# Kernel optimization log

Measured on AMD Instinct MI355X. Metric: run time of the kernel, lower is better.

The kernel has to match this reference:

```python
import jax, jax.numpy as jnp
import numpy as np

# FP4 (e2m1) value table: sign bit in code>>3, magnitude in code&7
FP4 = jnp.array([0.0, 0.5, 1.0, 1.5, 2.0, 3.0, 4.0, 6.0,
                 -0.0, -0.5, -1.0, -1.5, -2.0, -3.0, -4.0, -6.0], dtype=jnp.float32)
BLOCK = 32  # MX block size: one shared E8M0 scale per 32 elements


def _unpack(packed):
    # packed: int32 holding byte values 0..255; low nibble first
    lo = packed & 0xF
    hi = (packed >> 4) & 0xF
    return jnp.stack([lo, hi], axis=-1).reshape(*packed.shape[:-1], packed.shape[-1] * 2)


def _dequant(packed, sf):
    # packed: [..., N//2] packed FP4 codes; sf: [..., N//32] E8M0 exponents
    vals = FP4[_unpack(packed)]                       # [..., N]
    n = vals.shape[-1]
    scale = jnp.exp2(sf.astype(jnp.float32) - 127.0)  # [..., N//32]
    vals = vals.reshape(*vals.shape[:-1], n // BLOCK, BLOCK) * scale[..., None]
    return vals.reshape(*scale.shape[:-1], n)


def setup_inputs() -> dict:
    key = jax.random.key(0)
    ks = jax.random.split(key, 6)
    M, IN, OUT, R = 8192, 4096, 4096, 128
    return {
        "x_q": jax.random.randint(ks[0], (M, IN // 2), 0, 256, dtype=jnp.int32),
        "scales_x": jax.random.randint(ks[1], (M, IN // BLOCK), 120, 134, dtype=jnp.int32),
        "weight": jax.random.randint(ks[2], (OUT, IN // 2), 0, 256, dtype=jnp.int32),
        "SF_w": jax.random.randint(ks[3], (OUT * IN // BLOCK,), 120, 134, dtype=jnp.int32),
        "low_rank_weight": jax.random.randint(ks[4], (OUT, R // 2), 0, 256, dtype=jnp.int32),
        "SF_low_rank_weight": jax.random.randint(ks[5], (OUT * R // BLOCK,), 120, 134, dtype=jnp.int32),
    }


def reference(x_q, scales_x, weight, SF_w, low_rank_weight, SF_low_rank_weight):
    OUT = weight.shape[0]
    IN = weight.shape[1] * 2
    R = low_rank_weight.shape[1] * 2  # 128
    # Low-rank path: first R unpacked features of x (R//2 packed bytes, R//32 scale blocks)
    x_lr = _dequant(x_q[:, :R // 2], scales_x[:, :R // BLOCK])                    # [M, R]
    W_lr = _dequant(low_rank_weight, SF_low_rank_weight.reshape(OUT, R // BLOCK))  # [OUT, R]
    out = jnp.einsum('mr,or->mo', x_lr, W_lr, preferred_element_type=jnp.float32)
    # Main 4-bit matmul fused with the low-rank correction
    x = _dequant(x_q, scales_x)                               # [M, IN]
    W = _dequant(weight, SF_w.reshape(OUT, IN // BLOCK))      # [OUT, IN]
    out = out + jnp.einsum('mi,oi->mo', x, W, preferred_element_type=jnp.float32)
    return out
```

## Files before the change

kernel.cpp:

```cpp
#include <hip/hip_runtime.h>
#include <hip/hip_bf16.h>
#include <stdint.h>


#define M_DIM 8192
#define N_DIM 4096
#define K_MAIN 4096
#define K_TOT 4224
#define NCHUNK 132
#define NT 33

#define XP_OFF   ((size_t)0)
#define WP_OFF   (XP_OFF + (size_t)NCHUNK * M_DIM * 16)
#define SXH_OFF  (WP_OFF + (size_t)NCHUNK * N_DIM * 16)
#define SWH_OFF  (SXH_OFF + (size_t)NT * 2 * M_DIM * 2)
#define WS_NEED  (SWH_OFF + (size_t)NT * 2 * N_DIM * 2)

typedef __attribute__((ext_vector_type(4))) float f32x4;
typedef __attribute__((ext_vector_type(16))) float f32x16;
typedef __attribute__((ext_vector_type(8))) short short8;
typedef __attribute__((ext_vector_type(8))) _Float16 half8;
typedef __attribute__((ext_vector_type(4))) int i32x4;
typedef __attribute__((ext_vector_type(8))) int i32x8;

#define SBAR() asm volatile("s_barrier" ::: "memory")

#define PXP_N (NCHUNK * M_DIM)
#define PWP_N (NCHUNK * N_DIM)
#define TSX_N (NT * 2 * M_DIM / 2)
#define TSW_N (NT * 2 * N_DIM / 2)
#define PACK_TOTAL (PXP_N + PWP_N + TSX_N + TSW_N)

__device__ inline unsigned pack4(i32x4 q) {
    return (q.x & 255) | ((q.y & 255) << 8) | ((q.z & 255) << 16) |
           ((unsigned)(q.w & 255) << 24);
}

__global__ __launch_bounds__(256)
void pack_kernel(const int* __restrict__ xq, const int* __restrict__ sx,
                 const int* __restrict__ w, const int* __restrict__ sfw,
                 const int* __restrict__ lrw, const int* __restrict__ sflr,
                 uint8_t* __restrict__ ws) {
    int t = blockIdx.x * 256 + threadIdx.x;
    if (t < PXP_N) {
        const int g = t >> 13;
        const int m = t & 8191;
        const int gs = (g < 128) ? g : (g - 128);
        const int* src = xq + (size_t)m * 2048 + gs * 16;
        i32x4 o;
        o.x = (int)pack4(*(const i32x4*)(src + 0));
        o.y = (int)pack4(*(const i32x4*)(src + 4));
        o.z = (int)pack4(*(const i32x4*)(src + 8));
        o.w = (int)pack4(*(const i32x4*)(src + 12));
        *(i32x4*)(ws + XP_OFF + ((size_t)g * M_DIM + m) * 16) = o;
    } else if (t < PXP_N + PWP_N) {
        const int i = t - PXP_N;
        const int g = i >> 12;
        const int n = i & 4095;
        const int* src = (g < 128) ? (w + (size_t)n * 2048 + g * 16)
                                   : (lrw + (size_t)n * 64 + (g - 128) * 16);
        i32x4 o;
        o.x = (int)pack4(*(const i32x4*)(src + 0));
        o.y = (int)pack4(*(const i32x4*)(src + 4));
        o.z = (int)pack4(*(const i32x4*)(src + 8));
        o.w = (int)pack4(*(const i32x4*)(src + 12));
        *(i32x4*)(ws + WP_OFF + ((size_t)g * N_DIM + n) * 16) = o;
    } else if (t < PXP_N + PWP_N + TSX_N) {
        int i = t - PXP_N - PWP_N;
        int plane = i >> 12;
        int kt = plane >> 1, h = plane & 1;
        int r2 = (i & 4095) << 1;
        int g0 = kt * 4 + h, g2 = g0 + 2;
        int s0 = (g0 < 128) ? g0 : g0 - 128;
        int s2 = (g2 < 128) ? g2 : g2 - 128;
        unsigned b0 = sx[(size_t)r2 * 128 + s0] & 255;
        unsigned b1 = sx[(size_t)r2 * 128 + s2] & 255;
        unsigned b2 = sx[(size_t)(r2 + 1) * 128 + s0] & 255;
        unsigned b3 = sx[(size_t)(r2 + 1) * 128 + s2] & 255;
        *(unsigned*)(ws + SXH_OFF + (size_t)i * 4) = b0 | (b1 << 8) | (b2 << 16) | (b3 << 24);
    } else if (t < PACK_TOTAL) {
        int i = t - PXP_N - PWP_N - TSX_N;
        int plane = i >> 11;
        int kt = plane >> 1, h = plane & 1;
        int r2 = (i & 2047) << 1;
        int g0 = kt * 4 + h, g2 = g0 + 2;
        unsigned b0, b1, b2, b3;
        if (g0 < 128) { b0 = sfw[(size_t)r2 * 128 + g0] & 255; b2 = sfw[(size_t)(r2 + 1) * 128 + g0] & 255; }
        else          { b0 = sflr[(size_t)r2 * 4 + (g0 - 128)] & 255; b2 = sflr[(size_t)(r2 + 1) * 4 + (g0 - 128)] & 255; }
        if (g2 < 128) { b1 = sfw[(size_t)r2 * 128 + g2] & 255; b3 = sfw[(size_t)(r2 + 1) * 128 + g2] & 255; }
        else          { b1 = sflr[(size_t)r2 * 4 + (g2 - 128)] & 255; b3 = sflr[(size_t)(r2 + 1) * 4 + (g2 - 128)] & 255; }
        *(unsigned*)(ws + SWH_OFF + (size_t)i * 4) = b0 | (b1 << 8) | (b2 << 16) | (b3 << 24);
    }
}

__device__ inline void gload_lds16(const void* g, void* l) {
    __builtin_amdgcn_global_load_lds(
        (const __attribute__((address_space(1))) unsigned int*)g,
        (__attribute__((address_space(3))) unsigned int*)l, 16, 0, 0);
}

__device__ inline i32x8 zext8(i32x4 v) {
    return i32x8{v.x, v.y, v.z, v.w, 0, 0, 0, 0};
}

__global__ __launch_bounds__(512, 2)
void l4b_mx6(const uint8_t* __restrict__ xp, const uint8_t* __restrict__ wp,
             const uint8_t* __restrict__ sxH, const uint8_t* __restrict__ swH,
             float* __restrict__ out) {
    __shared__ __align__(16) uint8_t As[2][4][256][16];
    __shared__ __align__(16) uint8_t Bs[2][4][256][16];

    const int tid = threadIdx.x;
    const int lane = tid & 63;
    const int wid = tid >> 6;
    const int wr = wid >> 2;
    const int wc = wid & 3;

    const int bid = blockIdx.x;
    const int wgid = (bid & 7) * 64 + (bid >> 3);
    const int bn = (wgid & 15) * 256;
    const int bm = (wgid >> 4) * 256;

    const int h = lane >> 5, r = lane & 31;

    const int cst = wid & 3;
    const uint8_t* ga = (wid < 4)
        ? xp + ((size_t)cst * M_DIM + bm + lane) * 16
        : wp + ((size_t)cst * N_DIM + bn + lane) * 16;
    const size_t gstride = (wid < 4) ? (size_t)4 * M_DIM * 16 : (size_t)4 * N_DIM * 16;
    const uint8_t* psx = sxH + (size_t)(h * M_DIM + bm + wr * 128 + r) * 2;
    const uint8_t* psw = swH + (size_t)(h * N_DIM + bn + wc * 64 + r) * 2;
    const int laneoffA = h * 4096 + (wr * 128 + r) * 16;
    const int laneoffB = h * 4096 + (wc * 64 + r) * 16;

    f32x16 acc[4][2] = {};
    int sa[4], sb[2], san[4], sbn[2];

    {
        uint8_t(*T)[256][16] = (wid < 4) ? As[0] : Bs[0];
#pragma unroll
        for (int q = 0; q < 4; ++q)
            gload_lds16(ga + q * 1024, &T[cst][q * 64][0]);
        ga += gstride;
    }
#pragma unroll
    for (int mi = 0; mi < 4; ++mi) sa[mi] = *(const unsigned short*)(psx + mi * 64);
#pragma unroll
    for (int ni = 0; ni < 2; ++ni) sb[ni] = *(const unsigned short*)(psw + ni * 64);
    psx += 2 * M_DIM * 2;
    psw += 2 * N_DIM * 2;
    asm volatile("s_waitcnt vmcnt(0)" ::: "memory");
    SBAR();

    int cur = 0;
    for (int t = 0; t < NT; ++t) {
        const int nxt = cur ^ 1;

        if (t + 1 < NT) {
            uint8_t(*T)[256][16] = (wid < 4) ? As[nxt] : Bs[nxt];
#pragma unroll
            for (int q = 0; q < 4; ++q)
                gload_lds16(ga + q * 1024, &T[cst][q * 64][0]);
            ga += gstride;
#pragma unroll
            for (int mi = 0; mi < 4; ++mi) san[mi] = *(const unsigned short*)(psx + mi * 64);
#pragma unroll
            for (int ni = 0; ni < 2; ++ni) sbn[ni] = *(const unsigned short*)(psw + ni * 64);
            psx += 2 * M_DIM * 2;
            psw += 2 * N_DIM * 2;
        }

        const char* pa = (const char*)As + cur * 16384 + laneoffA;
        const char* pb = (const char*)Bs + cur * 16384 + laneoffB;
        i32x4 af0[4], af1[4], bf0[2], bf1[2];
#pragma unroll
        for (int mi = 0; mi < 4; ++mi) {
            af0[mi] = *(const i32x4*)(pa + mi * 512);
            af1[mi] = *(const i32x4*)(pa + 8192 + mi * 512);
        }
#pragma unroll
        for (int ni = 0; ni < 2; ++ni) {
            bf0[ni] = *(const i32x4*)(pb + ni * 512);
            bf1[ni] = *(const i32x4*)(pb + 8192 + ni * 512);
        }

        __builtin_amdgcn_s_setprio(1);
        {
            i32x8 a8[4], b8[2];
#pragma unroll
            for (int mi = 0; mi < 4; ++mi) a8[mi] = zext8(af0[mi]);
#pragma unroll
            for (int ni = 0; ni < 2; ++ni) b8[ni] = zext8(bf0[ni]);
#pragma unroll
            for (int mi = 0; mi < 4; ++mi)
#pragma unroll
                for (int ni = 0; ni < 2; ++ni)
                    acc[mi][ni] = __builtin_amdgcn_mfma_scale_f32_32x32x64_f8f6f4(
                        a8[mi], b8[ni], acc[mi][ni], 4, 4, 0, sa[mi], 0, sb[ni]);
        }
        {
            i32x8 a8[4], b8[2];
#pragma unroll
            for (int mi = 0; mi < 4; ++mi) a8[mi] = zext8(af1[mi]);
#pragma unroll
            for (int ni = 0; ni < 2; ++ni) b8[ni] = zext8(bf1[ni]);
#pragma unroll
            for (int mi = 0; mi < 4; ++mi)
#pragma unroll
                for (int ni = 0; ni < 2; ++ni)
                    acc[mi][ni] = __builtin_amdgcn_mfma_scale_f32_32x32x64_f8f6f4(
                        a8[mi], b8[ni], acc[mi][ni], 4, 4, 1, sa[mi], 1, sb[ni]);
        }
        __builtin_amdgcn_s_setprio(0);

        asm volatile("s_waitcnt vmcnt(0)" ::: "memory");
        SBAR();

        cur = nxt;
#pragma unroll
        for (int i = 0; i < 4; ++i) sa[i] = san[i];
        sb[0] = sbn[0]; sb[1] = sbn[1];
    }

#pragma unroll
    for (int mi = 0; mi < 4; ++mi)
#pragma unroll
        for (int ni = 0; ni < 2; ++ni) {
            const int col = bn + wc * 64 + ni * 32 + (lane & 31);
            const int rb = bm + wr * 128 + mi * 32 + 4 * (lane >> 5);
#pragma unroll
            for (int reg = 0; reg < 16; ++reg) {
                const int row = rb + (reg & 3) + 8 * (reg >> 2);
                out[(size_t)row * N_DIM + col] = acc[mi][ni][reg];
            }
        }
}

__device__ inline short8 dequant8_f16(i32x4 q, int sf) {
    unsigned b = (unsigned)q.x | ((unsigned)q.y << 8) |
                 ((unsigned)q.z << 16) | ((unsigned)q.w << 24);
    unsigned me = b & 0x07070707u;
    unsigned mo = (b >> 4) & 0x07070707u;
    const unsigned TLO = 0x3E3C3800u;
    const unsigned THI = 0x46444240u;
    unsigned He = __builtin_amdgcn_perm(THI, TLO, me);
    unsigned Ho = __builtin_amdgcn_perm(THI, TLO, mo);
    He |= (b & 0x08080808u) << 4;
    Ho |= (b & 0x80808080u);
    unsigned d0 = __builtin_amdgcn_perm(He, 0u, 0x05010400u);
    unsigned d1 = __builtin_amdgcn_perm(He, 0u, 0x07000600u);
    unsigned d2 = __builtin_amdgcn_perm(Ho, 0u, 0x05010400u);
    unsigned d3 = __builtin_amdgcn_perm(Ho, 0u, 0x07000600u);
    i32x4 di; di.x = (int)d0; di.y = (int)d1; di.z = (int)d2; di.w = (int)d3;
    half8 hh = __builtin_bit_cast(half8, di);
    unsigned short se = (unsigned short)((sf - 112) << 10);
    int srep = (int)((unsigned)se | ((unsigned)se << 16));
    i32x4 si; si.x = srep; si.y = srep; si.z = srep; si.w = srep;
    hh = hh * __builtin_bit_cast(half8, si);
    return __builtin_bit_cast(short8, hh);
}

__global__ __launch_bounds__(256)
void l4b_fused(const int* __restrict__ x_q, const int* __restrict__ scales_x,
               const int* __restrict__ weight, const int* __restrict__ SF_w,
               const int* __restrict__ lrw, const int* __restrict__ SF_lr,
               float* __restrict__ out) {
    __shared__ short As[128 * 64];
    __shared__ short Bs[128 * 64];
    const int tid = threadIdx.x;
    const int lane = tid & 63;
    const int wid = tid >> 6;
    const int wr = wid >> 1, wc = wid & 1;
    const int bm = blockIdx.y * 128, bn = blockIdx.x * 128;
    const int srow = tid >> 3;
    const int scol = (tid & 7) * 8;
    f32x4 acc[4][4] = {};
    for (int kt = 0; kt < K_TOT / 64; ++kt) {
        const int k0 = kt * 64;
        __syncthreads();
#pragma unroll
        for (int it = 0; it < 4; ++it) {
            const int row = it * 32 + srow;
            const int k = k0 + scol;
            const int ksrc = (k < K_MAIN) ? k : (k - K_MAIN);
            i32x4 q = *(const i32x4*)(x_q + (size_t)(bm + row) * 2048 + (ksrc >> 1));
            int sf = scales_x[(size_t)(bm + row) * 128 + (ksrc >> 5)];
            short8 v = dequant8_f16(q, sf);
            unsigned a = (unsigned)(row * 128 + scol * 2) ^ (unsigned)((row & 7) << 4);
            *(short8*)((char*)As + a) = v;
        }
#pragma unroll
        for (int it = 0; it < 4; ++it) {
            const int row = it * 32 + srow;
            const int k = k0 + scol;
            i32x4 q; int sf;
            if (k < K_MAIN) {
                q = *(const i32x4*)(weight + (size_t)(bn + row) * 2048 + (k >> 1));
                sf = SF_w[(size_t)(bn + row) * 128 + (k >> 5)];
            } else {
                q = *(const i32x4*)(lrw + (size_t)(bn + row) * 64 + ((k - K_MAIN) >> 1));
                sf = SF_lr[(size_t)(bn + row) * 4 + ((k - K_MAIN) >> 5)];
            }
            short8 v = dequant8_f16(q, sf);
            unsigned a = (unsigned)(row * 128 + scol * 2) ^ (unsigned)((row & 7) << 4);
            *(short8*)((char*)Bs + a) = v;
        }
        __syncthreads();
#pragma unroll
        for (int ks = 0; ks < 2; ++ks) {
            const int koff = ks * 32 + (lane >> 4) * 8;
            short8 af[4], bfr[4];
#pragma unroll
            for (int mi = 0; mi < 4; ++mi) {
                const int row = wr * 64 + mi * 16 + (lane & 15);
                unsigned a = (unsigned)(row * 128 + koff * 2) ^ (unsigned)((row & 7) << 4);
                af[mi] = *(const short8*)((const char*)As + a);
            }
#pragma unroll
            for (int ni = 0; ni < 4; ++ni) {
                const int row = wc * 64 + ni * 16 + (lane & 15);
                unsigned a = (unsigned)(row * 128 + koff * 2) ^ (unsigned)((row & 7) << 4);
                bfr[ni] = *(const short8*)((const char*)Bs + a);
            }
#pragma unroll
            for (int mi = 0; mi < 4; ++mi)
#pragma unroll
                for (int ni = 0; ni < 4; ++ni)
                    acc[mi][ni] = __builtin_amdgcn_mfma_f32_16x16x32_f16(
                        __builtin_bit_cast(half8, af[mi]),
                        __builtin_bit_cast(half8, bfr[ni]),
                        acc[mi][ni], 0, 0, 0);
        }
    }
#pragma unroll
    for (int mi = 0; mi < 4; ++mi)
#pragma unroll
        for (int ni = 0; ni < 4; ++ni) {
            const int col = bn + wc * 64 + ni * 16 + (lane & 15);
            const int row0 = bm + wr * 64 + mi * 16 + (lane >> 4) * 4;
#pragma unroll
            for (int r2 = 0; r2 < 4; ++r2)
                out[(size_t)(row0 + r2) * N_DIM + col] = acc[mi][ni][r2];
        }
}

extern "C" void kernel_launch(void* const* d_in, const int* in_sizes, int n_in,
                              void* d_out, int out_size, void* d_ws, size_t ws_size,
                              hipStream_t stream) {
    const int* x_q  = (const int*)d_in[0];
    const int* sx   = (const int*)d_in[1];
    const int* w    = (const int*)d_in[2];
    const int* sfw  = (const int*)d_in[3];
    const int* lrw  = (const int*)d_in[4];
    const int* sflr = (const int*)d_in[5];
    float* out = (float*)d_out;

    if (ws_size >= WS_NEED) {
        uint8_t* ws = (uint8_t*)d_ws;
        pack_kernel<<<(PACK_TOTAL + 255) / 256, 256, 0, stream>>>(x_q, sx, w, sfw, lrw, sflr, ws);
        l4b_mx6<<<(M_DIM / 256) * (N_DIM / 256), 512, 0, stream>>>(
            ws + XP_OFF, ws + WP_OFF, ws + SXH_OFF, ws + SWH_OFF, out);
    } else {
        dim3 grid(N_DIM / 128, M_DIM / 128);
        l4b_fused<<<grid, dim3(256), 0, stream>>>(x_q, sx, w, sfw, lrw, sflr, out);
    }
}
```

Measured before the change: 120.3 us.

## Load MX operands directly from global into registers, dropping LDS staging

The GEMM kernel no longer stages A and B tiles through double-buffered shared memory with global_load_lds and barriers. Each wave now loads its fragments and scales straight from global memory into registers every K step, then issues the scaled MFMAs. This removes the LDS traffic, the barriers and the shared-memory footprint. In exchange, each operand is fetched by several waves through cache instead of once per block, and there is no explicit prefetch to hide load latency. The zero-extend is also replaced by an undefined-upper shufflevector, and the occupancy hint in launch_bounds is dropped.

```diff
diff --git a/kernel.cpp b/kernel.cpp
--- a/kernel.cpp
+++ b/kernel.cpp
@@ -22,8 +22,6 @@
 typedef __attribute__((ext_vector_type(8))) _Float16 half8;
 typedef __attribute__((ext_vector_type(4))) int i32x4;
 typedef __attribute__((ext_vector_type(8))) int i32x8;
-
-#define SBAR() asm volatile("s_barrier" ::: "memory")
 
 #define PXP_N (NCHUNK * M_DIM)
 #define PWP_N (NCHUNK * N_DIM)
@@ -93,23 +91,14 @@
     }
 }
 
-__device__ inline void gload_lds16(const void* g, void* l) {
-    __builtin_amdgcn_global_load_lds(
-        (const __attribute__((address_space(1))) unsigned int*)g,
-        (__attribute__((address_space(3))) unsigned int*)l, 16, 0, 0);
-}
-
-__device__ inline i32x8 zext8(i32x4 v) {
-    return i32x8{v.x, v.y, v.z, v.w, 0, 0, 0, 0};
-}
-
-__global__ __launch_bounds__(512, 2)
-void l4b_mx6(const uint8_t* __restrict__ xp, const uint8_t* __restrict__ wp,
+__device__ inline i32x8 ext8(i32x4 v) {
+    return __builtin_shufflevector(v, v, 0, 1, 2, 3, -1, -1, -1, -1);
+}
+
+__global__ __launch_bounds__(512)
+void l4b_mx7(const uint8_t* __restrict__ xp, const uint8_t* __restrict__ wp,
              const uint8_t* __restrict__ sxH, const uint8_t* __restrict__ swH,
              float* __restrict__ out) {
-    __shared__ __align__(16) uint8_t As[2][4][256][16];
-    __shared__ __align__(16) uint8_t Bs[2][4][256][16];
-
     const int tid = threadIdx.x;
     const int lane = tid & 63;
     const int wid = tid >> 6;
@@ -123,103 +112,49 @@
 
     const int h = lane >> 5, r = lane & 31;
 
-    const int cst = wid & 3;
-    const uint8_t* ga = (wid < 4)
-        ? xp + ((size_t)cst * M_DIM + bm + lane) * 16
-        : wp + ((size_t)cst * N_DIM + bn + lane) * 16;
-    const size_t gstride = (wid < 4) ? (size_t)4 * M_DIM * 16 : (size_t)4 * N_DIM * 16;
-    const uint8_t* psx = sxH + (size_t)(h * M_DIM + bm + wr * 128 + r) * 2;
-    const uint8_t* psw = swH + (size_t)(h * N_DIM + bn + wc * 64 + r) * 2;
-    const int laneoffA = h * 4096 + (wr * 128 + r) * 16;
-    const int laneoffB = h * 4096 + (wc * 64 + r) * 16;
+    const uint8_t* pa = xp + ((size_t)h * M_DIM + bm + wr * 128 + r) * 16;
+    const uint8_t* pb = wp + ((size_t)h * N_DIM + bn + wc * 64 + r) * 16;
+    const uint8_t* psx = sxH + ((size_t)h * M_DIM + bm + wr * 128 + r) * 2;
+    const uint8_t* psw = swH + ((size_t)h * N_DIM + bn + wc * 64 + r) * 2;
+    const size_t paK = (size_t)2 * M_DIM * 16;
+    const size_t pbK = (size_t)2 * N_DIM * 16;
 
     f32x16 acc[4][2] = {};
-    int sa[4], sb[2], san[4], sbn[2];
-
-    {
-        uint8_t(*T)[256][16] = (wid < 4) ? As[0] : Bs[0];
-#pragma unroll
-        for (int q = 0; q < 4; ++q)
-            gload_lds16(ga + q * 1024, &T[cst][q * 64][0]);
-        ga += gstride;
-    }
-#pragma unroll
-    for (int mi = 0; mi < 4; ++mi) sa[mi] = *(const unsigned short*)(psx + mi * 64);
-#pragma unroll
-    for (int ni = 0; ni < 2; ++ni) sb[ni] = *(const unsigned short*)(psw + ni * 64);
-    psx += 2 * M_DIM * 2;
-    psw += 2 * N_DIM * 2;
-    asm volatile("s_waitcnt vmcnt(0)" ::: "memory");
-    SBAR();
-
-    int cur = 0;
+
     for (int t = 0; t < NT; ++t) {
-        const int nxt = cur ^ 1;
-
-        if (t + 1 < NT) {
-            uint8_t(*T)[256][16] = (wid < 4) ? As[nxt] : Bs[nxt];
-#pragma unroll
-            for (int q = 0; q < 4; ++q)
-                gload_lds16(ga + q * 1024, &T[cst][q * 64][0]);
-            ga += gstride;
-#pragma unroll
-            for (int mi = 0; mi < 4; ++mi) san[mi] = *(const unsigned short*)(psx + mi * 64);
-#pragma unroll
-            for (int ni = 0; ni < 2; ++ni) sbn[ni] = *(const unsigned short*)(psw + ni * 64);
-            psx += 2 * M_DIM * 2;
-            psw += 2 * N_DIM * 2;
-        }
-
-        const char* pa = (const char*)As + cur * 16384 + laneoffA;
-        const char* pb = (const char*)Bs + cur * 16384 + laneoffB;
         i32x4 af0[4], af1[4], bf0[2], bf1[2];
+        int sa[4], sb[2];
 #pragma unroll
         for (int mi = 0; mi < 4; ++mi) {
             af0[mi] = *(const i32x4*)(pa + mi * 512);
-            af1[mi] = *(const i32x4*)(pa + 8192 + mi * 512);
+            af1[mi] = *(const i32x4*)(pa + paK + mi * 512);
         }
 #pragma unroll
         for (int ni = 0; ni < 2; ++ni) {
             bf0[ni] = *(const i32x4*)(pb + ni * 512);
-            bf1[ni] = *(const i32x4*)(pb + 8192 + ni * 512);
-        }
-
-        __builtin_amdgcn_s_setprio(1);
-        {
-            i32x8 a8[4], b8[2];
-#pragma unroll
-            for (int mi = 0; mi < 4; ++mi) a8[mi] = zext8(af0[mi]);
-#pragma unroll
-            for (int ni = 0; ni < 2; ++ni) b8[ni] = zext8(bf0[ni]);
-#pragma unroll
-            for (int mi = 0; mi < 4; ++mi)
-#pragma unroll
-                for (int ni = 0; ni < 2; ++ni)
-                    acc[mi][ni] = __builtin_amdgcn_mfma_scale_f32_32x32x64_f8f6f4(
-                        a8[mi], b8[ni], acc[mi][ni], 4, 4, 0, sa[mi], 0, sb[ni]);
-        }
-        {
-            i32x8 a8[4], b8[2];
-#pragma unroll
-            for (int mi = 0; mi < 4; ++mi) a8[mi] = zext8(af1[mi]);
-#pragma unroll
-            for (int ni = 0; ni < 2; ++ni) b8[ni] = zext8(bf1[ni]);
-#pragma unroll
-            for (int mi = 0; mi < 4; ++mi)
-#pragma unroll
-                for (int ni = 0; ni < 2; ++ni)
-                    acc[mi][ni] = __builtin_amdgcn_mfma_scale_f32_32x32x64_f8f6f4(
-                        a8[mi], b8[ni], acc[mi][ni], 4, 4, 1, sa[mi], 1, sb[ni]);
-        }
-        __builtin_amdgcn_s_setprio(0);
-
-        asm volatile("s_waitcnt vmcnt(0)" ::: "memory");
-        SBAR();
-
-        cur = nxt;
-#pragma unroll
-        for (int i = 0; i < 4; ++i) sa[i] = san[i];
-        sb[0] = sbn[0]; sb[1] = sbn[1];
+            bf1[ni] = *(const i32x4*)(pb + pbK + ni * 512);
+        }
+#pragma unroll
+        for (int mi = 0; mi < 4; ++mi) sa[mi] = *(const unsigned short*)(psx + mi * 64);
+#pragma unroll
+        for (int ni = 0; ni < 2; ++ni) sb[ni] = *(const unsigned short*)(psw + ni * 64);
+        pa += (size_t)4 * M_DIM * 16;
+        pb += (size_t)4 * N_DIM * 16;
+        psx += (size_t)2 * M_DIM * 2;
+        psw += (size_t)2 * N_DIM * 2;
+
+#pragma unroll
+        for (int mi = 0; mi < 4; ++mi)
+#pragma unroll
+            for (int ni = 0; ni < 2; ++ni)
+                acc[mi][ni] = __builtin_amdgcn_mfma_scale_f32_32x32x64_f8f6f4(
+                    ext8(af0[mi]), ext8(bf0[ni]), acc[mi][ni], 4, 4, 0, sa[mi], 0, sb[ni]);
+#pragma unroll
+        for (int mi = 0; mi < 4; ++mi)
+#pragma unroll
+            for (int ni = 0; ni < 2; ++ni)
+                acc[mi][ni] = __builtin_amdgcn_mfma_scale_f32_32x32x64_f8f6f4(
+                    ext8(af1[mi]), ext8(bf1[ni]), acc[mi][ni], 4, 4, 1, sa[mi], 1, sb[ni]);
     }
 
 #pragma unroll
@@ -358,7 +293,7 @@
     if (ws_size >= WS_NEED) {
         uint8_t* ws = (uint8_t*)d_ws;
         pack_kernel<<<(PACK_TOTAL + 255) / 256, 256, 0, stream>>>(x_q, sx, w, sfw, lrw, sflr, ws);
-        l4b_mx6<<<(M_DIM / 256) * (N_DIM / 256), 512, 0, stream>>>(
+        l4b_mx7<<<(M_DIM / 256) * (N_DIM / 256), 512, 0, stream>>>(
             ws + XP_OFF, ws + WP_OFF, ws + SXH_OFF, ws + SWH_OFF, out);
     } else {
         dim3 grid(N_DIM / 128, M_DIM / 128);
```

Result: slower. 191.5 us (+59.2%).

## Triple-buffer LDS tiles with prefetch distance two in MX FP4 GEMM

Applied to the files above, without the earlier changes.

Moves the main GEMM loop from double to triple LDS buffering. Global-to-LDS loads are now issued two K-tiles ahead, and the wait becomes a partial vmcnt(4) that only drains the older tile, so more memory latency can be hidden behind MFMA work. It also replaces the zero-extension of MFMA operands with an undefined-upper shufflevector to save register moves. The cost is that shared memory per block grows from 64KB to 96KB. Two 512-thread blocks may then no longer fit on one CU, which would halve occupancy and leave the 512-block grid running in more waves.

```diff
diff --git a/kernel.cpp b/kernel.cpp
--- a/kernel.cpp
+++ b/kernel.cpp
@@ -99,16 +99,16 @@
         (__attribute__((address_space(3))) unsigned int*)l, 16, 0, 0);
 }
 
-__device__ inline i32x8 zext8(i32x4 v) {
-    return i32x8{v.x, v.y, v.z, v.w, 0, 0, 0, 0};
+__device__ inline i32x8 ext8(i32x4 v) {
+    return __builtin_shufflevector(v, v, 0, 1, 2, 3, -1, -1, -1, -1);
 }
 
 __global__ __launch_bounds__(512, 2)
-void l4b_mx6(const uint8_t* __restrict__ xp, const uint8_t* __restrict__ wp,
+void l4b_mx8(const uint8_t* __restrict__ xp, const uint8_t* __restrict__ wp,
              const uint8_t* __restrict__ sxH, const uint8_t* __restrict__ swH,
              float* __restrict__ out) {
-    __shared__ __align__(16) uint8_t As[2][4][256][16];
-    __shared__ __align__(16) uint8_t Bs[2][4][256][16];
+    __shared__ __align__(16) uint8_t As[3][4][256][16];
+    __shared__ __align__(16) uint8_t Bs[3][4][256][16];
 
     const int tid = threadIdx.x;
     const int lane = tid & 63;
@@ -139,8 +139,7 @@
     {
         uint8_t(*T)[256][16] = (wid < 4) ? As[0] : Bs[0];
 #pragma unroll
-        for (int q = 0; q < 4; ++q)
-            gload_lds16(ga + q * 1024, &T[cst][q * 64][0]);
+        for (int q = 0; q < 4; ++q) gload_lds16(ga + q * 1024, &T[cst][q * 64][0]);
         ga += gstride;
     }
 #pragma unroll
@@ -149,19 +148,18 @@
     for (int ni = 0; ni < 2; ++ni) sb[ni] = *(const unsigned short*)(psw + ni * 64);
     psx += 2 * M_DIM * 2;
     psw += 2 * N_DIM * 2;
-    asm volatile("s_waitcnt vmcnt(0)" ::: "memory");
+    {
+        uint8_t(*T)[256][16] = (wid < 4) ? As[1] : Bs[1];
+#pragma unroll
+        for (int q = 0; q < 4; ++q) gload_lds16(ga + q * 1024, &T[cst][q * 64][0]);
+        ga += gstride;
+    }
+    asm volatile("s_waitcnt vmcnt(4)" ::: "memory");
     SBAR();
 
-    int cur = 0;
+    int b0 = 0;
     for (int t = 0; t < NT; ++t) {
-        const int nxt = cur ^ 1;
-
         if (t + 1 < NT) {
-            uint8_t(*T)[256][16] = (wid < 4) ? As[nxt] : Bs[nxt];
-#pragma unroll
-            for (int q = 0; q < 4; ++q)
-                gload_lds16(ga + q * 1024, &T[cst][q * 64][0]);
-            ga += gstride;
 #pragma unroll
             for (int mi = 0; mi < 4; ++mi) san[mi] = *(const unsigned short*)(psx + mi * 64);
 #pragma unroll
@@ -169,9 +167,16 @@
             psx += 2 * M_DIM * 2;
             psw += 2 * N_DIM * 2;
         }
-
-        const char* pa = (const char*)As + cur * 16384 + laneoffA;
-        const char* pb = (const char*)Bs + cur * 16384 + laneoffB;
+        if (t + 2 < NT) {
+            int b2 = b0 + 2; if (b2 >= 3) b2 -= 3;
+            uint8_t(*T)[256][16] = (wid < 4) ? As[b2] : Bs[b2];
+#pragma unroll
+            for (int q = 0; q < 4; ++q) gload_lds16(ga + q * 1024, &T[cst][q * 64][0]);
+            ga += gstride;
+        }
+
+        const char* pa = (const char*)As + b0 * 16384 + laneoffA;
+        const char* pb = (const char*)Bs + b0 * 16384 + laneoffB;
         i32x4 af0[4], af1[4], bf0[2], bf1[2];
 #pragma unroll
         for (int mi = 0; mi < 4; ++mi) {
@@ -185,38 +190,28 @@
         }
 
         __builtin_amdgcn_s_setprio(1);
-        {
-            i32x8 a8[4], b8[2];
-#pragma unroll
-            for (int mi = 0; mi < 4; ++mi) a8[mi] = zext8(af0[mi]);
-#pragma unroll
-            for (int ni = 0; ni < 2; ++ni) b8[ni] = zext8(bf0[ni]);
-#pragma unroll
-            for (int mi = 0; mi < 4; ++mi)
-#pragma unroll
-                for (int ni = 0; ni < 2; ++ni)
-                    acc[mi][ni] = __builtin_amdgcn_mfma_scale_f32_32x32x64_f8f6f4(
-                        a8[mi], b8[ni], acc[mi][ni], 4, 4, 0, sa[mi], 0, sb[ni]);
-        }
-        {
-            i32x8 a8[4], b8[2];
-#pragma unroll
-            for (int mi = 0; mi < 4; ++mi) a8[mi] = zext8(af1[mi]);
-#pragma unroll
-            for (int ni = 0; ni < 2; ++ni) b8[ni] = zext8(bf1[ni]);
-#pragma unroll
-            for (int mi = 0; mi < 4; ++mi)
-#pragma unroll
-                for (int ni = 0; ni < 2; ++ni)
-                    acc[mi][ni] = __builtin_amdgcn_mfma_scale_f32_32x32x64_f8f6f4(
-                        a8[mi], b8[ni], acc[mi][ni], 4, 4, 1, sa[mi], 1, sb[ni]);
-        }
+#pragma unroll
+        for (int mi = 0; mi < 4; ++mi)
+#pragma unroll
+            for (int ni = 0; ni < 2; ++ni)
+                acc[mi][ni] = __builtin_amdgcn_mfma_scale_f32_32x32x64_f8f6f4(
+                    ext8(af0[mi]), ext8(bf0[ni]), acc[mi][ni], 4, 4, 0, sa[mi], 0, sb[ni]);
+#pragma unroll
+        for (int mi = 0; mi < 4; ++mi)
+#pragma unroll
+            for (int ni = 0; ni < 2; ++ni)
+                acc[mi][ni] = __builtin_amdgcn_mfma_scale_f32_32x32x64_f8f6f4(
+                    ext8(af1[mi]), ext8(bf1[ni]), acc[mi][ni], 4, 4, 1, sa[mi], 1, sb[ni]);
         __builtin_amdgcn_s_setprio(0);
 
-        asm volatile("s_waitcnt vmcnt(0)" ::: "memory");
+        if (t + 2 < NT) {
+            asm volatile("s_waitcnt vmcnt(4)" ::: "memory");
+        } else {
+            asm volatile("s_waitcnt vmcnt(0)" ::: "memory");
+        }
         SBAR();
 
-        cur = nxt;
+        b0 = (b0 == 2) ? 0 : b0 + 1;
 #pragma unroll
         for (int i = 0; i < 4; ++i) sa[i] = san[i];
         sb[0] = sbn[0]; sb[1] = sbn[1];
@@ -358,7 +353,7 @@
     if (ws_size >= WS_NEED) {
         uint8_t* ws = (uint8_t*)d_ws;
         pack_kernel<<<(PACK_TOTAL + 255) / 256, 256, 0, stream>>>(x_q, sx, w, sfw, lrw, sflr, ws);
-        l4b_mx6<<<(M_DIM / 256) * (N_DIM / 256), 512, 0, stream>>>(
+        l4b_mx8<<<(M_DIM / 256) * (N_DIM / 256), 512, 0, stream>>>(
             ws + XP_OFF, ws + WP_OFF, ws + SXH_OFF, ws + SWH_OFF, out);
     } else {
         dim3 grid(N_DIM / 128, M_DIM / 128);
```

New measurement: 120.8 us. About the same (+0.4%).

## Load B fragments directly from global into registers, drop B LDS staging

Applied to the files above, without the earlier changes.

The B (weight) operand is no longer staged through shared memory. Each wave now reads its own B fragments straight from global memory into registers and double-buffers them across iterations, while all 8 waves share the A tile loads into LDS. This halves LDS usage and LDS read traffic, and the zero-extension of the operands is replaced by an undefined-upper shufflevector. The cost is redundant global reads of B, since waves in different rows fetch the same data, plus extra register pressure from the prefetch buffers.

```diff
diff --git a/kernel.cpp b/kernel.cpp
--- a/kernel.cpp
+++ b/kernel.cpp
@@ -99,16 +99,15 @@
         (__attribute__((address_space(3))) unsigned int*)l, 16, 0, 0);
 }
 
-__device__ inline i32x8 zext8(i32x4 v) {
-    return i32x8{v.x, v.y, v.z, v.w, 0, 0, 0, 0};
+__device__ inline i32x8 ext8(i32x4 v) {
+    return __builtin_shufflevector(v, v, 0, 1, 2, 3, -1, -1, -1, -1);
 }
 
 __global__ __launch_bounds__(512, 2)
-void l4b_mx6(const uint8_t* __restrict__ xp, const uint8_t* __restrict__ wp,
-             const uint8_t* __restrict__ sxH, const uint8_t* __restrict__ swH,
-             float* __restrict__ out) {
+void l4b_mx10(const uint8_t* __restrict__ xp, const uint8_t* __restrict__ wp,
+              const uint8_t* __restrict__ sxH, const uint8_t* __restrict__ swH,
+              float* __restrict__ out) {
     __shared__ __align__(16) uint8_t As[2][4][256][16];
-    __shared__ __align__(16) uint8_t Bs[2][4][256][16];
 
     const int tid = threadIdx.x;
     const int lane = tid & 63;
@@ -123,26 +122,26 @@
 
     const int h = lane >> 5, r = lane & 31;
 
-    const int cst = wid & 3;
-    const uint8_t* ga = (wid < 4)
-        ? xp + ((size_t)cst * M_DIM + bm + lane) * 16
-        : wp + ((size_t)cst * N_DIM + bn + lane) * 16;
-    const size_t gstride = (wid < 4) ? (size_t)4 * M_DIM * 16 : (size_t)4 * N_DIM * 16;
+    const uint8_t* ga = xp + ((size_t)(wid >> 1) * M_DIM + bm + (wid & 1) * 128 + lane) * 16;
+    const int lds_base = (wid >> 1) * 4096 + (wid & 1) * 2048;
+    const uint8_t* pbg = wp + ((size_t)h * N_DIM + bn + wc * 64 + r) * 16;
     const uint8_t* psx = sxH + (size_t)(h * M_DIM + bm + wr * 128 + r) * 2;
     const uint8_t* psw = swH + (size_t)(h * N_DIM + bn + wc * 64 + r) * 2;
     const int laneoffA = h * 4096 + (wr * 128 + r) * 16;
-    const int laneoffB = h * 4096 + (wc * 64 + r) * 16;
 
     f32x16 acc[4][2] = {};
     int sa[4], sb[2], san[4], sbn[2];
-
-    {
-        uint8_t(*T)[256][16] = (wid < 4) ? As[0] : Bs[0];
-#pragma unroll
-        for (int q = 0; q < 4; ++q)
-            gload_lds16(ga + q * 1024, &T[cst][q * 64][0]);
-        ga += gstride;
-    }
+    i32x4 bc[2][2], bnx[2][2];
+
+    gload_lds16(ga, (char*)As + lds_base);
+    gload_lds16(ga + 1024, (char*)As + lds_base + 1024);
+    ga += (size_t)4 * M_DIM * 16;
+#pragma unroll
+    for (int kk = 0; kk < 2; ++kk)
+#pragma unroll
+        for (int ni = 0; ni < 2; ++ni)
+            bc[kk][ni] = *(const i32x4*)(pbg + kk * ((size_t)2 * N_DIM * 16) + ni * 512);
+    pbg += (size_t)4 * N_DIM * 16;
 #pragma unroll
     for (int mi = 0; mi < 4; ++mi) sa[mi] = *(const unsigned short*)(psx + mi * 64);
 #pragma unroll
@@ -154,14 +153,17 @@
 
     int cur = 0;
     for (int t = 0; t < NT; ++t) {
-        const int nxt = cur ^ 1;
-
         if (t + 1 < NT) {
-            uint8_t(*T)[256][16] = (wid < 4) ? As[nxt] : Bs[nxt];
-#pragma unroll
-            for (int q = 0; q < 4; ++q)
-                gload_lds16(ga + q * 1024, &T[cst][q * 64][0]);
-            ga += gstride;
+            char* db = (char*)As + (cur ^ 1) * 16384 + lds_base;
+            gload_lds16(ga, db);
+            gload_lds16(ga + 1024, db + 1024);
+            ga += (size_t)4 * M_DIM * 16;
+#pragma unroll
+            for (int kk = 0; kk < 2; ++kk)
+#pragma unroll
+                for (int ni = 0; ni < 2; ++ni)
+                    bnx[kk][ni] = *(const i32x4*)(pbg + kk * ((size_t)2 * N_DIM * 16) + ni * 512);
+            pbg += (size_t)4 * N_DIM * 16;
 #pragma unroll
             for (int mi = 0; mi < 4; ++mi) san[mi] = *(const unsigned short*)(psx + mi * 64);
 #pragma unroll
@@ -171,52 +173,36 @@
         }
 
         const char* pa = (const char*)As + cur * 16384 + laneoffA;
-        const char* pb = (const char*)Bs + cur * 16384 + laneoffB;
-        i32x4 af0[4], af1[4], bf0[2], bf1[2];
+        i32x4 af0[4], af1[4];
 #pragma unroll
         for (int mi = 0; mi < 4; ++mi) {
             af0[mi] = *(const i32x4*)(pa + mi * 512);
             af1[mi] = *(const i32x4*)(pa + 8192 + mi * 512);
         }
-#pragma unroll
-        for (int ni = 0; ni < 2; ++ni) {
-            bf0[ni] = *(const i32x4*)(pb + ni * 512);
-            bf1[ni] = *(const i32x4*)(pb + 8192 + ni * 512);
-        }
 
         __builtin_amdgcn_s_setprio(1);
-        {
-            i32x8 a8[4], b8[2];
-#pragma unroll
-            for (int mi = 0; mi < 4; ++mi) a8[mi] = zext8(af0[mi]);
-#pragma unroll
-            for (int ni = 0; ni < 2; ++ni) b8[ni] = zext8(bf0[ni]);
-#pragma unroll
-            for (int mi = 0; mi < 4; ++mi)
-#pragma unroll
-                for (int ni = 0; ni < 2; ++ni)
-                    acc[mi][ni] = __builtin_amdgcn_mfma_scale_f32_32x32x64_f8f6f4(
-                        a8[mi], b8[ni], acc[mi][ni], 4, 4, 0, sa[mi], 0, sb[ni]);
-        }
-        {
-            i32x8 a8[4], b8[2];
-#pragma unroll
-            for (int mi = 0; mi < 4; ++mi) a8[mi] = zext8(af1[mi]);
-#pragma unroll
-            for (int ni = 0; ni < 2; ++ni) b8[ni] = zext8(bf1[ni]);
-#pragma unroll
-            for (int mi = 0; mi < 4; ++mi)
-#pragma unroll
-                for (int ni = 0; ni < 2; ++ni)
-                    acc[mi][ni] = __builtin_amdgcn_mfma_scale_f32_32x32x64_f8f6f4(
-                        a8[mi], b8[ni], acc[mi][ni], 4, 4, 1, sa[mi], 1, sb[ni]);
-        }
+#pragma unroll
+        for (int mi = 0; mi < 4; ++mi)
+#pragma unroll
+            for (int ni = 0; ni < 2; ++ni)
+                acc[mi][ni] = __builtin_amdgcn_mfma_scale_f32_32x32x64_f8f6f4(
+                    ext8(af0[mi]), ext8(bc[0][ni]), acc[mi][ni], 4, 4, 0, sa[mi], 0, sb[ni]);
+#pragma unroll
+        for (int mi = 0; mi < 4; ++mi)
+#pragma unroll
+            for (int ni = 0; ni < 2; ++ni)
+                acc[mi][ni] = __builtin_amdgcn_mfma_scale_f32_32x32x64_f8f6f4(
+                    ext8(af1[mi]), ext8(bc[1][ni]), acc[mi][ni], 4, 4, 1, sa[mi], 1, sb[ni]);
         __builtin_amdgcn_s_setprio(0);
 
         asm volatile("s_waitcnt vmcnt(0)" ::: "memory");
         SBAR();
 
-        cur = nxt;
+        cur ^= 1;
+#pragma unroll
+        for (int kk = 0; kk < 2; ++kk)
+#pragma unroll
+            for (int ni = 0; ni < 2; ++ni) bc[kk][ni] = bnx[kk][ni];
 #pragma unroll
         for (int i = 0; i < 4; ++i) sa[i] = san[i];
         sb[0] = sbn[0]; sb[1] = sbn[1];
@@ -358,7 +344,7 @@
     if (ws_size >= WS_NEED) {
         uint8_t* ws = (uint8_t*)d_ws;
         pack_kernel<<<(PACK_TOTAL + 255) / 256, 256, 0, stream>>>(x_q, sx, w, sfw, lrw, sflr, ws);
-        l4b_mx6<<<(M_DIM / 256) * (N_DIM / 256), 512, 0, stream>>>(
+        l4b_mx10<<<(M_DIM / 256) * (N_DIM / 256), 512, 0, stream>>>(
             ws + XP_OFF, ws + WP_OFF, ws + SXH_OFF, ws + SWH_OFF, out);
     } else {
         dim3 grid(N_DIM / 128, M_DIM / 128);
```

Result: slower. 123.3 us (+2.5%).
